# Kernel tuning notes

Measured on AMD Instinct MI355X. Metric: run time of the kernel, lower is better.

Reference implementation:

```python
import jax, jax.numpy as jnp
import numpy as np

N, D, H, C = 50000, 128, 4, 16  # nodes, in_dim, heads, out per head
E, ED = 800000, 64              # edges, edge feature dim
NEG_SLOPE = 0.2


def setup_inputs() -> dict:
    key = jax.random.key(0)
    ks = jax.random.split(key, 10)
    x = jax.random.normal(ks[0], (N, D), dtype=jnp.float32)
    edge_index = jax.random.randint(ks[1], (2, E), 0, N, dtype=jnp.int64)
    edge_attr = jax.random.normal(ks[2], (E, ED), dtype=jnp.float32)
    s = 0.1
    W = jax.random.normal(ks[3], (H * C, D), dtype=jnp.float32) * s       # lin (no bias)
    W_edge = jax.random.normal(ks[4], (H * C, ED), dtype=jnp.float32) * s  # lin_edge (no bias)
    att_src = jax.random.normal(ks[5], (H, C), dtype=jnp.float32) * s
    att_dst = jax.random.normal(ks[6], (H, C), dtype=jnp.float32) * s
    att_edge = jax.random.normal(ks[7], (H, C), dtype=jnp.float32) * s
    bias = jnp.zeros((H * C,), dtype=jnp.float32)
    return dict(x=x, edge_index=edge_index, edge_attr=edge_attr, W=W,
                W_edge=W_edge, att_src=att_src, att_dst=att_dst,
                att_edge=att_edge, bias=bias)


def reference(x, edge_index, edge_attr, W, W_edge, att_src, att_dst, att_edge, bias):
    n = x.shape[0]
    src0, dst0 = edge_index[0], edge_index[1]

    # PyG GATConv default: add self-loops, self-loop edge_attr = per-dst mean of incoming edge_attr
    ones = jnp.ones((src0.shape[0],), dtype=edge_attr.dtype)
    cnt = jax.ops.segment_sum(ones, dst0, num_segments=n)                # [N]
    loop_attr = jax.ops.segment_sum(edge_attr, dst0, num_segments=n)
    loop_attr = loop_attr / jnp.maximum(cnt, 1.0)[:, None]               # [N, ED]
    ar = jnp.arange(n, dtype=src0.dtype)
    src = jnp.concatenate([src0, ar])
    dst = jnp.concatenate([dst0, ar])
    ea = jnp.concatenate([edge_attr, loop_attr], axis=0)                 # [E+N, ED]

    xh = (x @ W.T).reshape(n, H, C)                                      # [N, H, C]
    a_src = jnp.einsum('nhc,hc->nh', xh, att_src)                        # [N, H]
    a_dst = jnp.einsum('nhc,hc->nh', xh, att_dst)
    eh = (ea @ W_edge.T).reshape(-1, H, C)                               # [E+N, H, C]
    a_edge = jnp.einsum('ehc,hc->eh', eh, att_edge)                      # [E+N, H]

    alpha = a_src[src] + a_dst[dst] + a_edge                             # [E+N, H]
    alpha = jax.nn.leaky_relu(alpha, NEG_SLOPE)

    # softmax over edges grouped by destination node (PyG softmax)
    amax = jax.ops.segment_max(alpha, dst, num_segments=n)               # [N, H]
    alpha = jnp.exp(alpha - amax[dst])
    denom = jax.ops.segment_sum(alpha, dst, num_segments=n)
    alpha = alpha / (denom[dst] + 1e-16)

    # message = x_j * alpha, scatter-add to destination
    out = jax.ops.segment_sum(xh[src] * alpha[:, :, None], dst, num_segments=n)  # [N,H,C]
    return out.reshape(n, H * C) + bias
```

## Files before the change

### kernel.cpp

```cpp
#include <hip/hip_runtime.h>
#include <math.h>

#define N_NODES 50000
#define DIM     128
#define NHEAD   4
#define NCH     16
#define HC      64
#define NE      800000
#define EDIM    64
#define NEG     0.2f
#define MAXE    64

__device__ __forceinline__ float lrelu(float v) { return v > 0.f ? v : NEG * v; }

__global__ void k1_vedge(const float* __restrict__ W_edge, const float* __restrict__ att_edge,
                         float* __restrict__ v_edge) {
    int t = threadIdx.x;
    int h = t >> 6, d = t & 63;
    float acc = 0.f;
    #pragma unroll
    for (int c = 0; c < NCH; ++c)
        acc = fmaf(att_edge[h * NCH + c], W_edge[(h * NCH + c) * EDIM + d], acc);
    v_edge[h * 64 + d] = acc;
}

__global__ __launch_bounds__(256) void k2_xh(const float* __restrict__ x, const float* __restrict__ W,
                                             const float* __restrict__ att_src, const float* __restrict__ att_dst,
                                             float* __restrict__ xh, float* __restrict__ a_src,
                                             float* __restrict__ a_dst) {
    __shared__ float Wt[128 * 68];
    int t = threadIdx.x;
    for (int idx = t; idx < 64 * 128; idx += 256) {
        int col = idx >> 7, k = idx & 127;
        Wt[k * 68 + col] = W[idx];
    }
    __syncthreads();

    int h  = t & 3;
    int rp = t >> 2;
    int row0 = blockIdx.x * 128 + rp * 2;
    int r0 = min(row0, N_NODES - 1);
    int r1 = min(row0 + 1, N_NODES - 1);
    const float4* x0 = (const float4*)(x + (size_t)r0 * DIM);
    const float4* x1 = (const float4*)(x + (size_t)r1 * DIM);

    float acc0[16], acc1[16];
    #pragma unroll
    for (int c = 0; c < 16; ++c) { acc0[c] = 0.f; acc1[c] = 0.f; }

    for (int k4 = 0; k4 < 32; ++k4) {
        float4 xa = x0[k4];
        float4 xb = x1[k4];
        #pragma unroll
        for (int kk = 0; kk < 4; ++kk) {
            float va = (&xa.x)[kk];
            float vb = (&xb.x)[kk];
            const float* wr = &Wt[(k4 * 4 + kk) * 68 + h * 16];
            #pragma unroll
            for (int j = 0; j < 4; ++j) {
                float4 w = *(const float4*)(wr + 4 * j);
                acc0[4 * j + 0] = fmaf(va, w.x, acc0[4 * j + 0]);
                acc0[4 * j + 1] = fmaf(va, w.y, acc0[4 * j + 1]);
                acc0[4 * j + 2] = fmaf(va, w.z, acc0[4 * j + 2]);
                acc0[4 * j + 3] = fmaf(va, w.w, acc0[4 * j + 3]);
                acc1[4 * j + 0] = fmaf(vb, w.x, acc1[4 * j + 0]);
                acc1[4 * j + 1] = fmaf(vb, w.y, acc1[4 * j + 1]);
                acc1[4 * j + 2] = fmaf(vb, w.z, acc1[4 * j + 2]);
                acc1[4 * j + 3] = fmaf(vb, w.w, acc1[4 * j + 3]);
            }
        }
    }

    if (row0 < N_NODES) {
        float4* o = (float4*)(xh + (size_t)row0 * HC + h * 16);
        o[0] = make_float4(acc0[0], acc0[1], acc0[2], acc0[3]);
        o[1] = make_float4(acc0[4], acc0[5], acc0[6], acc0[7]);
        o[2] = make_float4(acc0[8], acc0[9], acc0[10], acc0[11]);
        o[3] = make_float4(acc0[12], acc0[13], acc0[14], acc0[15]);
        float ss = 0.f, sd = 0.f;
        #pragma unroll
        for (int c = 0; c < 16; ++c) {
            ss = fmaf(acc0[c], att_src[h * 16 + c], ss);
            sd = fmaf(acc0[c], att_dst[h * 16 + c], sd);
        }
        a_src[row0 * 4 + h] = ss;
        a_dst[row0 * 4 + h] = sd;
    }
    if (row0 + 1 < N_NODES) {
        float4* o = (float4*)(xh + (size_t)(row0 + 1) * HC + h * 16);
        o[0] = make_float4(acc1[0], acc1[1], acc1[2], acc1[3]);
        o[1] = make_float4(acc1[4], acc1[5], acc1[6], acc1[7]);
        o[2] = make_float4(acc1[8], acc1[9], acc1[10], acc1[11]);
        o[3] = make_float4(acc1[12], acc1[13], acc1[14], acc1[15]);
        float ss = 0.f, sd = 0.f;
        #pragma unroll
        for (int c = 0; c < 16; ++c) {
            ss = fmaf(acc1[c], att_src[h * 16 + c], ss);
            sd = fmaf(acc1[c], att_dst[h * 16 + c], sd);
        }
        a_src[(row0 + 1) * 4 + h] = ss;
        a_dst[(row0 + 1) * 4 + h] = sd;
    }
}

__global__ __launch_bounds__(256) void kp_edge(const float* __restrict__ edge_attr,
                                               const int* __restrict__ ei,
                                               const float* __restrict__ v_edge,
                                               float* __restrict__ p_e,
                                               int* __restrict__ deg) {
    int lane = threadIdx.x & 63;
    int q = lane & 15;
    float4 w0 = *(const float4*)(v_edge + 0 * 64 + q * 4);
    float4 w1 = *(const float4*)(v_edge + 1 * 64 + q * 4);
    float4 w2 = *(const float4*)(v_edge + 2 * 64 + q * 4);
    float4 w3 = *(const float4*)(v_edge + 3 * 64 + q * 4);

    int wave   = (blockIdx.x * 256 + threadIdx.x) >> 6;
    int nwaves = gridDim.x * 4;
    for (int g = wave; g < NE / 4; g += nwaves) {
        float4 v = *(const float4*)(edge_attr + (size_t)g * 256 + lane * 4);
        float p0 = fmaf(v.x, w0.x, fmaf(v.y, w0.y, fmaf(v.z, w0.z, v.w * w0.w)));
        float p1 = fmaf(v.x, w1.x, fmaf(v.y, w1.y, fmaf(v.z, w1.z, v.w * w1.w)));
        float p2 = fmaf(v.x, w2.x, fmaf(v.y, w2.y, fmaf(v.z, w2.z, v.w * w2.w)));
        float p3 = fmaf(v.x, w3.x, fmaf(v.y, w3.y, fmaf(v.z, w3.z, v.w * w3.w)));
        #pragma unroll
        for (int m = 1; m < 16; m <<= 1) {
            p0 += __shfl_xor(p0, m);
            p1 += __shfl_xor(p1, m);
            p2 += __shfl_xor(p2, m);
            p3 += __shfl_xor(p3, m);
        }
        int e = g * 4 + (lane >> 4);
        if (q < 4) {
            float pv = (q == 0) ? p0 : (q == 1) ? p1 : (q == 2) ? p2 : p3;
            p_e[(size_t)e * 4 + q] = pv;
        }
        if (q == 0)
            atomicAdd(deg + ei[NE + e], 1);
    }
}

__global__ void k4a_scan(const int* __restrict__ deg, int* __restrict__ tmp, int* __restrict__ bsums) {
    int t = threadIdx.x;
    int i = blockIdx.x * 256 + t;
    int v = (i < N_NODES) ? deg[i] : 0;
    int lane = t & 63, w = t >> 6;
    int xv = v;
    #pragma unroll
    for (int o = 1; o < 64; o <<= 1) {
        int y = __shfl_up(xv, o);
        if (lane >= o) xv += y;
    }
    __shared__ int wtot[4];
    if (lane == 63) wtot[w] = xv;
    __syncthreads();
    int add = 0;
    #pragma unroll
    for (int j = 0; j < 4; ++j)
        if (j < w) add += wtot[j];
    xv += add;
    if (i < N_NODES) tmp[i] = xv;
    if (t == 255) bsums[blockIdx.x] = xv;
}

__global__ void k4b_scan(int* __restrict__ bsums, int nb) {
    int t = threadIdx.x;
    int v = (t < nb) ? bsums[t] : 0;
    int lane = t & 63, w = t >> 6;
    int xv = v;
    #pragma unroll
    for (int o = 1; o < 64; o <<= 1) {
        int y = __shfl_up(xv, o);
        if (lane >= o) xv += y;
    }
    __shared__ int wtot[4];
    if (lane == 63) wtot[w] = xv;
    __syncthreads();
    int add = 0;
    #pragma unroll
    for (int j = 0; j < 4; ++j)
        if (j < w) add += wtot[j];
    xv += add;
    if (t < nb) bsums[t] = xv - v;
}

__global__ void k4c_finish(const int* __restrict__ tmp, const int* __restrict__ bsums,
                           const int* __restrict__ deg, int* __restrict__ rowptr,
                           int* __restrict__ cursor) {
    int i = blockIdx.x * 256 + threadIdx.x;
    if (i >= N_NODES) return;
    int incl = tmp[i] + bsums[i >> 8];
    rowptr[i + 1] = incl;
    cursor[i] = incl - deg[i];
    if (i == 0) rowptr[0] = 0;
}

__global__ __launch_bounds__(256) void k5_perm(const int* __restrict__ ei,
                                               int* __restrict__ cursor,
                                               int* __restrict__ perm) {
    int e = blockIdx.x * 256 + threadIdx.x;
    if (e >= NE) return;
    int dst = ei[NE + e];
    int pos = atomicAdd(cursor + dst, 1);
    perm[pos] = e;
}

__global__ __launch_bounds__(256) void k6_agg(const int* __restrict__ rowptr,
                                              const int* __restrict__ perm,
                                              const int* __restrict__ ei,
                                              const float* __restrict__ p_e,
                                              const float* __restrict__ xh,
                                              const float* __restrict__ a_src,
                                              const float* __restrict__ a_dst,
                                              const float* __restrict__ bias,
                                              float* __restrict__ out) {
    __shared__ __align__(16) float s_w[4][MAXE][4];
    __shared__ int s_src[4][MAXE];
    int wid  = threadIdx.x >> 6;
    int lane = threadIdx.x & 63;
    int n = blockIdx.x * 4 + wid;
    int start = rowptr[n], end = rowptr[n + 1];
    int degn = end - start;
    int m = min(degn, MAXE);

    for (int i = lane; i < m; i += 64) {
        int e = perm[start + i];
        s_src[wid][i] = ei[e];
        *(float4*)&s_w[wid][i][0] = *(const float4*)(p_e + (size_t)e * 4);
    }
    __syncthreads();

    int h = lane & 3;
    float adh = a_dst[n * 4 + h];
    float sw = 0.f, sp = 0.f;
    for (int i = lane >> 2; i < m; i += 16) {
        int s   = s_src[wid][i];
        float p = s_w[wid][i][h];
        float w = __expf(lrelu(a_src[(size_t)s * 4 + h] + adh + p));
        s_w[wid][i][h] = w;
        sw += w;
        sp += p;
    }
    for (int i = MAXE + (lane >> 2); i < degn; i += 16) {
        int e = perm[start + i];
        int s = ei[e];
        float p = p_e[(size_t)e * 4 + h];
        sw += __expf(lrelu(a_src[(size_t)s * 4 + h] + adh + p));
        sp += p;
    }
    sw += __shfl_xor(sw, 4);  sp += __shfl_xor(sp, 4);
    sw += __shfl_xor(sw, 8);  sp += __shfl_xor(sp, 8);
    sw += __shfl_xor(sw, 16); sp += __shfl_xor(sp, 16);
    sw += __shfl_xor(sw, 32); sp += __shfl_xor(sp, 32);

    float al    = sp / fmaxf((float)degn, 1.f);
    float wself = __expf(lrelu(a_src[n * 4 + h] + adh + al));
    float denom = sw + wself + 1e-16f;
    __syncthreads();

    int h2 = lane >> 4;
    float d2   = __shfl(denom, h2);
    float ws2  = __shfl(wself, h2);
    float adh2 = __shfl(adh, h2);
    float acc = ws2 * xh[(size_t)n * HC + lane];

    int i = 0;
    for (; i + 4 <= m; i += 4) {
        int s0 = s_src[wid][i], s1 = s_src[wid][i + 1];
        int s2 = s_src[wid][i + 2], s3 = s_src[wid][i + 3];
        float w0 = s_w[wid][i][h2],     w1 = s_w[wid][i + 1][h2];
        float w2 = s_w[wid][i + 2][h2], w3 = s_w[wid][i + 3][h2];
        float x0 = xh[(size_t)s0 * HC + lane];
        float x1 = xh[(size_t)s1 * HC + lane];
        float x2 = xh[(size_t)s2 * HC + lane];
        float x3 = xh[(size_t)s3 * HC + lane];
        acc = fmaf(w0, x0, acc);
        acc = fmaf(w1, x1, acc);
        acc = fmaf(w2, x2, acc);
        acc = fmaf(w3, x3, acc);
    }
    for (; i < m; ++i) {
        int s = s_src[wid][i];
        acc = fmaf(s_w[wid][i][h2], xh[(size_t)s * HC + lane], acc);
    }
    for (int j = MAXE; j < degn; ++j) {
        int e = perm[start + j];
        int s = ei[e];
        float p = p_e[(size_t)e * 4 + h2];
        float w = __expf(lrelu(a_src[(size_t)s * 4 + h2] + adh2 + p));
        acc = fmaf(w, xh[(size_t)s * HC + lane], acc);
    }
    out[(size_t)n * HC + lane] = acc / d2 + bias[lane];
}

extern "C" void kernel_launch(void* const* d_in, const int* in_sizes, int n_in,
                              void* d_out, int out_size, void* d_ws, size_t ws_size,
                              hipStream_t stream) {
    const float* x         = (const float*)d_in[0];
    const int*   ei        = (const int*)d_in[1];
    const float* edge_attr = (const float*)d_in[2];
    const float* W         = (const float*)d_in[3];
    const float* W_edge    = (const float*)d_in[4];
    const float* att_src   = (const float*)d_in[5];
    const float* att_dst   = (const float*)d_in[6];
    const float* att_edge  = (const float*)d_in[7];
    const float* bias      = (const float*)d_in[8];
    float* out = (float*)d_out;

    char* ws = (char*)d_ws;
    size_t off = 0;
    float* v_edge    = (float*)(ws + off); off += 1024;
    float* xh        = (float*)(ws + off); off += (size_t)N_NODES * HC * 4;
    float* a_src     = (float*)(ws + off); off += (size_t)N_NODES * 4 * 4;
    float* a_dst     = (float*)(ws + off); off += (size_t)N_NODES * 4 * 4;
    int*   deg       = (int*)(ws + off);   off += (size_t)N_NODES * 4;
    int*   tmp       = (int*)(ws + off);   off += (size_t)N_NODES * 4;
    int*   bsums     = (int*)(ws + off);   off += 1024;
    int*   rowptr    = (int*)(ws + off);   off += (size_t)(N_NODES + 4) * 4;
    int*   cursor    = (int*)(ws + off);   off += (size_t)N_NODES * 4;
    int*   perm      = (int*)(ws + off);   off += (size_t)NE * 4;
    float* p_e       = (float*)(ws + off); off += (size_t)NE * 4 * 4;

    hipMemsetAsync(deg, 0, (size_t)N_NODES * 4, stream);

    k1_vedge<<<1, 256, 0, stream>>>(W_edge, att_edge, v_edge);
    k2_xh<<<(N_NODES + 127) / 128, 256, 0, stream>>>(x, W, att_src, att_dst, xh, a_src, a_dst);
    kp_edge<<<1024, 256, 0, stream>>>(edge_attr, ei, v_edge, p_e, deg);
    int nb = (N_NODES + 255) / 256;
    k4a_scan<<<nb, 256, 0, stream>>>(deg, tmp, bsums);
    k4b_scan<<<1, 256, 0, stream>>>(bsums, nb);
    k4c_finish<<<nb, 256, 0, stream>>>(tmp, bsums, deg, rowptr, cursor);
    k5_perm<<<(NE + 255) / 256, 256, 0, stream>>>(ei, cursor, perm);
    k6_agg<<<N_NODES / 4, 256, 0, stream>>>(rowptr, perm, ei, p_e, xh,
                                            a_src, a_dst, bias, out);
}
```

Before: 472.2 us.

## Scatter edge logits and sources directly into CSR order, drop perm indirection

```diff
diff --git a/kernel.cpp b/kernel.cpp
--- a/kernel.cpp
+++ b/kernel.cpp
@@ -103,11 +103,73 @@
     }
 }
 
-__global__ __launch_bounds__(256) void kp_edge(const float* __restrict__ edge_attr,
-                                               const int* __restrict__ ei,
-                                               const float* __restrict__ v_edge,
-                                               float* __restrict__ p_e,
-                                               int* __restrict__ deg) {
+__global__ __launch_bounds__(256) void ka_deg(const int* __restrict__ ei, int* __restrict__ deg) {
+    int e = blockIdx.x * 256 + threadIdx.x;
+    if (e >= NE) return;
+    atomicAdd(deg + ei[NE + e], 1);
+}
+
+__global__ void k4a_scan(const int* __restrict__ deg, int* __restrict__ tmp, int* __restrict__ bsums) {
+    int t = threadIdx.x;
+    int i = blockIdx.x * 256 + t;
+    int v = (i < N_NODES) ? deg[i] : 0;
+    int lane = t & 63, w = t >> 6;
+    int xv = v;
+    #pragma unroll
+    for (int o = 1; o < 64; o <<= 1) {
+        int y = __shfl_up(xv, o);
+        if (lane >= o) xv += y;
+    }
+    __shared__ int wtot[4];
+    if (lane == 63) wtot[w] = xv;
+    __syncthreads();
+    int add = 0;
+    #pragma unroll
+    for (int j = 0; j < 4; ++j)
+        if (j < w) add += wtot[j];
+    xv += add;
+    if (i < N_NODES) tmp[i] = xv;
+    if (t == 255) bsums[blockIdx.x] = xv;
+}
+
+__global__ void k4b_scan(int* __restrict__ bsums, int nb) {
+    int t = threadIdx.x;
+    int v = (t < nb) ? bsums[t] : 0;
+    int lane = t & 63, w = t >> 6;
+    int xv = v;
+    #pragma unroll
+    for (int o = 1; o < 64; o <<= 1) {
+        int y = __shfl_up(xv, o);
+        if (lane >= o) xv += y;
+    }
+    __shared__ int wtot[4];
+    if (lane == 63) wtot[w] = xv;
+    __syncthreads();
+    int add = 0;
+    #pragma unroll
+    for (int j = 0; j < 4; ++j)
+        if (j < w) add += wtot[j];
+    xv += add;
+    if (t < nb) bsums[t] = xv - v;
+}
+
+__global__ void k4c_finish(const int* __restrict__ tmp, const int* __restrict__ bsums,
+                           const int* __restrict__ deg, int* __restrict__ rowptr,
+                           int* __restrict__ cursor) {
+    int i = blockIdx.x * 256 + threadIdx.x;
+    if (i >= N_NODES) return;
+    int incl = tmp[i] + bsums[i >> 8];
+    rowptr[i + 1] = incl;
+    cursor[i] = incl - deg[i];
+    if (i == 0) rowptr[0] = 0;
+}
+
+__global__ __launch_bounds__(256) void kp_csr(const float* __restrict__ edge_attr,
+                                              const int* __restrict__ ei,
+                                              const float* __restrict__ v_edge,
+                                              int* __restrict__ cursor,
+                                              int* __restrict__ csr_src,
+                                              float* __restrict__ csr_p) {
     int lane = threadIdx.x & 63;
     int q = lane & 15;
     float4 w0 = *(const float4*)(v_edge + 0 * 64 + q * 4);
@@ -130,85 +192,20 @@
             p2 += __shfl_xor(p2, m);
             p3 += __shfl_xor(p3, m);
         }
-        int e = g * 4 + (lane >> 4);
-        if (q < 4) {
-            float pv = (q == 0) ? p0 : (q == 1) ? p1 : (q == 2) ? p2 : p3;
-            p_e[(size_t)e * 4 + q] = pv;
-        }
-        if (q == 0)
-            atomicAdd(deg + ei[NE + e], 1);
-    }
-}
-
-__global__ void k4a_scan(const int* __restrict__ deg, int* __restrict__ tmp, int* __restrict__ bsums) {
-    int t = threadIdx.x;
-    int i = blockIdx.x * 256 + t;
-    int v = (i < N_NODES) ? deg[i] : 0;
-    int lane = t & 63, w = t >> 6;
-    int xv = v;
-    #pragma unroll
-    for (int o = 1; o < 64; o <<= 1) {
-        int y = __shfl_up(xv, o);
-        if (lane >= o) xv += y;
-    }
-    __shared__ int wtot[4];
-    if (lane == 63) wtot[w] = xv;
-    __syncthreads();
-    int add = 0;
-    #pragma unroll
-    for (int j = 0; j < 4; ++j)
-        if (j < w) add += wtot[j];
-    xv += add;
-    if (i < N_NODES) tmp[i] = xv;
-    if (t == 255) bsums[blockIdx.x] = xv;
-}
-
-__global__ void k4b_scan(int* __restrict__ bsums, int nb) {
-    int t = threadIdx.x;
-    int v = (t < nb) ? bsums[t] : 0;
-    int lane = t & 63, w = t >> 6;
-    int xv = v;
-    #pragma unroll
-    for (int o = 1; o < 64; o <<= 1) {
-        int y = __shfl_up(xv, o);
-        if (lane >= o) xv += y;
-    }
-    __shared__ int wtot[4];
-    if (lane == 63) wtot[w] = xv;
-    __syncthreads();
-    int add = 0;
-    #pragma unroll
-    for (int j = 0; j < 4; ++j)
-        if (j < w) add += wtot[j];
-    xv += add;
-    if (t < nb) bsums[t] = xv - v;
-}
-
-__global__ void k4c_finish(const int* __restrict__ tmp, const int* __restrict__ bsums,
-                           const int* __restrict__ deg, int* __restrict__ rowptr,
-                           int* __restrict__ cursor) {
-    int i = blockIdx.x * 256 + threadIdx.x;
-    if (i >= N_NODES) return;
-    int incl = tmp[i] + bsums[i >> 8];
-    rowptr[i + 1] = incl;
-    cursor[i] = incl - deg[i];
-    if (i == 0) rowptr[0] = 0;
-}
-
-__global__ __launch_bounds__(256) void k5_perm(const int* __restrict__ ei,
-                                               int* __restrict__ cursor,
-                                               int* __restrict__ perm) {
-    int e = blockIdx.x * 256 + threadIdx.x;
-    if (e >= NE) return;
-    int dst = ei[NE + e];
-    int pos = atomicAdd(cursor + dst, 1);
-    perm[pos] = e;
+        if (q == 0) {
+            int e = g * 4 + (lane >> 4);
+            int src = ei[e];
+            int dst = ei[NE + e];
+            int pos = atomicAdd(cursor + dst, 1);
+            csr_src[pos] = src;
+            *(float4*)(csr_p + (size_t)pos * 4) = make_float4(p0, p1, p2, p3);
+        }
+    }
 }
 
 __global__ __launch_bounds__(256) void k6_agg(const int* __restrict__ rowptr,
-                                              const int* __restrict__ perm,
-                                              const int* __restrict__ ei,
-                                              const float* __restrict__ p_e,
+                                              const int* __restrict__ csr_src,
+                                              const float* __restrict__ csr_p,
                                               const float* __restrict__ xh,
                                               const float* __restrict__ a_src,
                                               const float* __restrict__ a_dst,
@@ -224,9 +221,8 @@
     int m = min(degn, MAXE);
 
     for (int i = lane; i < m; i += 64) {
-        int e = perm[start + i];
-        s_src[wid][i] = ei[e];
-        *(float4*)&s_w[wid][i][0] = *(const float4*)(p_e + (size_t)e * 4);
+        s_src[wid][i] = csr_src[start + i];
+        *(float4*)&s_w[wid][i][0] = *(const float4*)(csr_p + (size_t)(start + i) * 4);
     }
     __syncthreads();
 
@@ -242,9 +238,8 @@
         sp += p;
     }
     for (int i = MAXE + (lane >> 2); i < degn; i += 16) {
-        int e = perm[start + i];
-        int s = ei[e];
-        float p = p_e[(size_t)e * 4 + h];
+        int s = csr_src[start + i];
+        float p = csr_p[(size_t)(start + i) * 4 + h];
         sw += __expf(lrelu(a_src[(size_t)s * 4 + h] + adh + p));
         sp += p;
     }
@@ -284,9 +279,8 @@
         acc = fmaf(s_w[wid][i][h2], xh[(size_t)s * HC + lane], acc);
     }
     for (int j = MAXE; j < degn; ++j) {
-        int e = perm[start + j];
-        int s = ei[e];
-        float p = p_e[(size_t)e * 4 + h2];
+        int s = csr_src[start + j];
+        float p = csr_p[(size_t)(start + j) * 4 + h2];
         float w = __expf(lrelu(a_src[(size_t)s * 4 + h2] + adh2 + p));
         acc = fmaf(w, xh[(size_t)s * HC + lane], acc);
     }
@@ -318,19 +312,19 @@
     int*   bsums     = (int*)(ws + off);   off += 1024;
     int*   rowptr    = (int*)(ws + off);   off += (size_t)(N_NODES + 4) * 4;
     int*   cursor    = (int*)(ws + off);   off += (size_t)N_NODES * 4;
-    int*   perm      = (int*)(ws + off);   off += (size_t)NE * 4;
-    float* p_e       = (float*)(ws + off); off += (size_t)NE * 4 * 4;
+    int*   csr_src   = (int*)(ws + off);   off += (size_t)NE * 4;
+    float* csr_p     = (float*)(ws + off); off += (size_t)NE * 4 * 4;
 
     hipMemsetAsync(deg, 0, (size_t)N_NODES * 4, stream);
 
     k1_vedge<<<1, 256, 0, stream>>>(W_edge, att_edge, v_edge);
     k2_xh<<<(N_NODES + 127) / 128, 256, 0, stream>>>(x, W, att_src, att_dst, xh, a_src, a_dst);
-    kp_edge<<<1024, 256, 0, stream>>>(edge_attr, ei, v_edge, p_e, deg);
+    ka_deg<<<(NE + 255) / 256, 256, 0, stream>>>(ei, deg);
     int nb = (N_NODES + 255) / 256;
     k4a_scan<<<nb, 256, 0, stream>>>(deg, tmp, bsums);
     k4b_scan<<<1, 256, 0, stream>>>(bsums, nb);
     k4c_finish<<<nb, 256, 0, stream>>>(tmp, bsums, deg, rowptr, cursor);
-    k5_perm<<<(NE + 255) / 256, 256, 0, stream>>>(ei, cursor, perm);
-    k6_agg<<<N_NODES / 4, 256, 0, stream>>>(rowptr, perm, ei, p_e, xh,
+    kp_csr<<<1024, 256, 0, stream>>>(edge_attr, ei, v_edge, cursor, csr_src, csr_p);
+    k6_agg<<<N_NODES / 4, 256, 0, stream>>>(rowptr, csr_src, csr_p, xh,
                                             a_src, a_dst, bias, out);
 }
```

Measured after the change: 466.1 us. Within noise of the previous version (-1.3%).
